# Kernel optimization log

Hardware: AMD Instinct MI355X
Metric: run time of the kernel (lower is better)

## Reference

```python
import jax, jax.numpy as jnp
import numpy as np

B, L, H, NHEADS = 32, 1024, 128, 2
HEAD = H // NHEADS
NEG = -2.0**32 + 1.0  # padding value used by the torch module


def setup_inputs() -> dict:
    key = jax.random.key(0)
    ks = jax.random.split(key, 9)
    queries = jax.random.normal(ks[0], (B, L, H), dtype=jnp.float32)
    keys = jax.random.normal(ks[1], (B, L, H), dtype=jnp.float32)
    time_mask = jax.random.bernoulli(ks[2], 0.1, (B, L))
    # causal mask: True above the diagonal (future positions masked)
    attn_mask = jnp.triu(jnp.ones((L, L), dtype=bool), k=1)
    s = 1.0 / np.sqrt(H)
    Qw = jax.random.uniform(ks[3], (H, H), jnp.float32, -s, s)
    Qb = jax.random.uniform(ks[4], (H,), jnp.float32, -s, s)
    Kw = jax.random.uniform(ks[5], (H, H), jnp.float32, -s, s)
    Kb = jax.random.uniform(ks[6], (H,), jnp.float32, -s, s)
    Vw = jax.random.uniform(ks[7], (H, H), jnp.float32, -s, s)
    Vb = jax.random.uniform(ks[8], (H,), jnp.float32, -s, s)
    return {"queries": queries, "keys": keys, "time_mask": time_mask,
            "attn_mask": attn_mask, "Qw": Qw, "Qb": Qb, "Kw": Kw, "Kb": Kb,
            "Vw": Vw, "Vb": Vb}


def reference(queries, keys, time_mask, attn_mask, Qw, Qb, Kw, Kb, Vw, Vb):
    b, l, h = queries.shape
    d = h // NHEADS
    # torch Linear: x @ W.T + b
    Q = queries @ Qw.T + Qb
    K = keys @ Kw.T + Kb
    V = keys @ Vw.T + Vb
    # split heads: torch cat(split(dim=2), dim=0) == (h, B, L, d) layout;
    # equivalent per-head math with (B, h, L, d):
    Qh = Q.reshape(b, l, NHEADS, d).transpose(0, 2, 1, 3)  # bhld
    Kh = K.reshape(b, l, NHEADS, d).transpose(0, 2, 1, 3)
    Vh = V.reshape(b, l, NHEADS, d).transpose(0, 2, 1, 3)
    scores = jnp.einsum('bhqd,bhkd->bhqk', Qh, Kh) / jnp.sqrt(
        jnp.asarray(d, dtype=Qh.dtype))
    # time_mask masks whole query rows; attn_mask is causal over (q, k)
    scores = jnp.where(time_mask[:, None, :, None], NEG, scores)
    scores = jnp.where(attn_mask[None, None, :, :], NEG, scores)
    attn = jax.nn.softmax(scores, axis=-1)  # dropout_rate=0 -> identity
    out = jnp.einsum('bhqk,bhkd->bhqd', attn, Vh)
    return out.transpose(0, 2, 1, 3).reshape(b, l, h)
```

## Files before the change

kernel.cpp:

```cpp
#include <hip/hip_runtime.h>

#define LSEQ 1024
#define DH 64
#define NH 2

typedef __attribute__((ext_vector_type(8))) __bf16 bf16x8;
typedef __attribute__((ext_vector_type(4))) float f32x4;
typedef __attribute__((ext_vector_type(8))) unsigned short ushort8;

__device__ __forceinline__ unsigned short f2bf(float f) {
  unsigned u = __float_as_uint(f);
  u += 0x7FFFu + ((u >> 16) & 1u);
  return (unsigned short)(u >> 16);
}
__device__ __forceinline__ unsigned cvt_pk_bf16(float lo, float hi) {
  unsigned r;
  asm("v_cvt_pk_bf16_f32 %0, %1, %2" : "=v"(r) : "v"(lo), "v"(hi));
  return r;
}
__device__ __forceinline__ void gload16(const void* g, void* l) {
  __builtin_amdgcn_global_load_lds(
      (const __attribute__((address_space(1))) void*)g,
      (__attribute__((address_space(3))) void*)l, 16, 0, 0);
}

#define QSCALE 0.1803368801111601f

__global__ __launch_bounds__(256) void wconv_kernel(
    const float* __restrict__ Qw, const float* __restrict__ Kw,
    const float* __restrict__ Vw, unsigned short* __restrict__ Wbf,
    float* __restrict__ Vmean)
{
  for (int i = blockIdx.x * 256 + threadIdx.x; i < NH * 32 * DH; i += 768)
    Vmean[i] = 0.f;
  const float* W = (blockIdx.x == 0) ? Qw : (blockIdx.x == 1) ? Kw : Vw;
  unsigned short* o = Wbf + blockIdx.x * 16384;
  const float4* W4 = (const float4*)W;
#pragma unroll
  for (int i = 0; i < 16; ++i) {
    const int idx = threadIdx.x + i * 256;
    const float4 v = W4[idx];
    uint2 u;
    u.x = cvt_pk_bf16(v.x, v.y);
    u.y = cvt_pk_bf16(v.z, v.w);
    *(uint2*)&o[idx * 4] = u;
  }
}

__global__ __launch_bounds__(256, 2) void proj_kernel(
    const float* __restrict__ queries, const float* __restrict__ keys,
    const unsigned short* __restrict__ Wbf,
    const float* __restrict__ Qb, const float* __restrict__ Kb,
    const float* __restrict__ Vb,
    unsigned short* __restrict__ Qbf, unsigned short* __restrict__ Kbf,
    unsigned short* __restrict__ Vt, float* __restrict__ Vmean)
{
  constexpr int LP = 136;
  __shared__ __align__(16) unsigned short Xs[128 * LP];
  __shared__ __align__(16) unsigned short Ws[16384];

  const int t = threadIdx.x;
  const int lane = t & 63, w = t >> 6;
  const int c = lane & 15, g = lane >> 4;
  const int wrow = w * 32;

  const int mat = blockIdx.x & 1;
  const int rt  = (blockIdx.x >> 1) * 128;

  const float* Xin = mat ? keys : queries;

#define WSTAGE(wi) do {                                                    \
    const char* Wg_ = (const char*)(Wbf + (wi) * 16384);                   \
    _Pragma("unroll")                                                      \
    for (int i_ = 0; i_ < 8; ++i_) {                                       \
      const int off_ = t * 16 + i_ * 4096;                                 \
      const int sch_ = ((((off_ >> 4) & 15) ^ ((off_ >> 8) & 7)) << 4);    \
      gload16(Wg_ + (off_ & ~0xFF) + sch_,                                 \
              (char*)Ws + w * 1024 + i_ * 4096);                           \
    }                                                                      \
  } while (0)

#define WFRAG(ct_, kc_) \
  (*(const bf16x8*)&Ws[((ct_) * 16 + c) * 128 + ((((kc_) * 4 + g) ^ (c & 7)) << 3)])

#define XFRAG(half_, kc_) \
  (*(const bf16x8*)&Xs[(wrow + (half_) * 16 + c) * LP + (kc_) * 32 + g * 8])

  WSTAGE(mat);

  const float4* X4 = (const float4*)(Xin + (size_t)rt * 128);
#pragma unroll
  for (int i = 0; i < 16; ++i) {
    const int e4 = t + i * 256;
    const float4 v = X4[e4];
    const int e = e4 * 4;
    uint2 u;
    u.x = cvt_pk_bf16(v.x, v.y);
    u.y = cvt_pk_bf16(v.z, v.w);
    *(uint2*)&Xs[(e >> 7) * LP + (e & 127)] = u;
  }
  __syncthreads();

  f32x4 accA[2][8];
#pragma unroll
  for (int i = 0; i < 2; ++i)
#pragma unroll
    for (int j = 0; j < 8; ++j) accA[i][j] = (f32x4){0.f, 0.f, 0.f, 0.f};

#pragma unroll
  for (int kc = 0; kc < 4; ++kc) {
    const bf16x8 a0 = XFRAG(0, kc);
    const bf16x8 a1 = XFRAG(1, kc);
#pragma unroll
    for (int ct = 0; ct < 8; ++ct) {
      const bf16x8 bfr = WFRAG(ct, kc);
      accA[0][ct] = __builtin_amdgcn_mfma_f32_16x16x32_bf16(a0, bfr, accA[0][ct], 0, 0, 0);
      accA[1][ct] = __builtin_amdgcn_mfma_f32_16x16x32_bf16(a1, bfr, accA[1][ct], 0, 0, 0);
    }
  }

  f32x4 accB[2][8];
  if (mat) {
    __syncthreads();
    WSTAGE(2);
    __syncthreads();

#pragma unroll
    for (int i = 0; i < 2; ++i)
#pragma unroll
      for (int j = 0; j < 8; ++j) accB[i][j] = (f32x4){0.f, 0.f, 0.f, 0.f};

#pragma unroll
    for (int kc = 0; kc < 4; ++kc) {
      const bf16x8 a0 = XFRAG(0, kc);
      const bf16x8 a1 = XFRAG(1, kc);
#pragma unroll
      for (int ct = 0; ct < 8; ++ct) {
        const bf16x8 bfr = WFRAG(ct, kc);
        accB[0][ct] = __builtin_amdgcn_mfma_f32_16x16x32_bf16(a0, bfr, accB[0][ct], 0, 0, 0);
        accB[1][ct] = __builtin_amdgcn_mfma_f32_16x16x32_bf16(a1, bfr, accB[1][ct], 0, 0, 0);
      }
    }

#pragma unroll
    for (int ct = 0; ct < 8; ++ct) {
      const float bv = Vb[ct * 16 + c];
      float cs = 8.f * bv;
#pragma unroll
      for (int qf = 0; qf < 2; ++qf)
#pragma unroll
        for (int r = 0; r < 4; ++r) cs += accB[qf][ct][r];
      cs += __shfl_xor(cs, 16);
      cs += __shfl_xor(cs, 32);
      if (g == 0) {
        const int col = ct * 16 + c;
        const int bh = (rt >> 10) * NH + (col >> 6);
        atomicAdd(&Vmean[bh * DH + (col & 63)], cs);
      }
    }
  }

  __syncthreads();
  {
    const float* biasA = mat ? Kb : Qb;
    const float qs = mat ? 1.0f : QSCALE;
#pragma unroll
    for (int qf = 0; qf < 2; ++qf)
#pragma unroll
      for (int ct = 0; ct < 8; ++ct) {
        const float bv = biasA[ct * 16 + c];
#pragma unroll
        for (int r = 0; r < 4; ++r)
          Xs[(wrow + qf * 16 + g * 4 + r) * LP + ct * 16 + c] =
              f2bf((accA[qf][ct][r] + bv) * qs);
      }
  }
  __syncthreads();
  {
    unsigned short* outp = (mat ? Kbf : Qbf) + (size_t)rt * 128;
#pragma unroll
    for (int i = 0; i < 8; ++i) {
      const int e = i * 2048 + t * 8;
      *(ushort8*)&outp[e] = *(const ushort8*)&Xs[(e >> 7) * LP + (e & 127)];
    }
  }

  if (mat) {
    __syncthreads();
#pragma unroll
    for (int qf = 0; qf < 2; ++qf)
#pragma unroll
      for (int ct = 0; ct < 8; ++ct) {
        const float bv = Vb[ct * 16 + c];
        const int col = ct * 16 + c;
        uint2 u;
        u.x = cvt_pk_bf16(accB[qf][ct][0] + bv, accB[qf][ct][1] + bv);
        u.y = cvt_pk_bf16(accB[qf][ct][2] + bv, accB[qf][ct][3] + bv);
        *(uint2*)&Xs[col * LP + wrow + qf * 16 + g * 4] = u;
      }
    __syncthreads();
    const int b = rt >> 10, l0 = rt & 1023;
#pragma unroll
    for (int i = 0; i < 8; ++i) {
      const int e = i * 2048 + t * 8;
      const int col = e >> 7, li = e & 127;
      const ushort8 v8 = *(const ushort8*)&Xs[col * LP + li];
      const int hh = col >> 6, dh = col & 63;
      unsigned short* vp = Vt + ((size_t)(b * NH + hh)) * (DH * LSEQ) +
                           (size_t)dh * LSEQ + l0 + li;
      *(ushort8*)vp = v8;
    }
  }
#undef WSTAGE
#undef WFRAG
#undef XFRAG
}

__global__ __launch_bounds__(256, 3) void attn_kernel(
    const unsigned short* __restrict__ Qbf, const unsigned short* __restrict__ Kbf,
    const unsigned short* __restrict__ Vt, const float* __restrict__ Vmean,
    const int* __restrict__ time_mask, float* __restrict__ out)
{
  __shared__ __align__(16) unsigned short smem[24576];

  const int tid = threadIdx.x;
  const int lane = tid & 63, w = tid >> 6;
  const int c = lane & 15, g = lane >> 4;

  const int wgid = blockIdx.x;
  const int xcd = wgid & 7;
  const int idx = wgid >> 3;
  const int bh  = xcd * 8 + (idx & 7);
  const int qb  = 7 - (idx >> 3);
  const int qbase = qb * 128;
  const int b = bh >> 1, h = bh & 1;

  const unsigned short* Qp = Qbf + ((size_t)b * LSEQ) * 128 + h * 64;
  const char* Kpb = (const char*)(Kbf + ((size_t)b * LSEQ) * 128 + h * 64);
  const char* Vpb = (const char*)(Vt + (size_t)bh * (DH * LSEQ));

  const int nkv = qb * 2 + 2;
  const int tkmax = qb * 2 + (w >> 1);

#define STAGE(tkv, bi) do {                                                   \
    const int kv_ = (tkv) * 64;                                               \
    _Pragma("unroll")                                                         \
    for (int r_ = 0; r_ < 2; ++r_) {                                          \
      const int off_ = tid * 16 + r_ * 4096;                                  \
      const int row_ = off_ >> 7;                                             \
      const int chk_ = (((off_ >> 4) & 7) ^ (row_ & 7)) << 4;                 \
      gload16(Kpb + (size_t)(kv_ + row_) * 256 + chk_,                        \
              (char*)smem + (bi) * 8192 + w * 1024 + r_ * 4096);              \
      gload16(Vpb + (size_t)row_ * 2048 + kv_ * 2 + chk_,                     \
              (char*)smem + 16384 + (bi) * 8192 + w * 1024 + r_ * 4096);      \
    }                                                                         \
  } while (0)

  bf16x8 qa[2][2];
#pragma unroll
  for (int qf = 0; qf < 2; ++qf)
#pragma unroll
    for (int kc = 0; kc < 2; ++kc)
      qa[qf][kc] = *(const bf16x8*)&Qp[(qbase + w * 32 + qf * 16 + c) * 128 + kc * 32 + g * 8];

  const __bf16 one = (__bf16)1.0f;
  const bf16x8 vones = {one, one, one, one, one, one, one, one};

  f32x4 acc[2][4];
  f32x4 acc5[2];
#pragma unroll
  for (int qf = 0; qf < 2; ++qf) {
    acc5[qf] = (f32x4){0.f, 0.f, 0.f, 0.f};
#pragma unroll
    for (int i = 0; i < 4; ++i) acc[qf][i] = (f32x4){0.f, 0.f, 0.f, 0.f};
  }

  unsigned short* const Pw = smem + 16384 + w * 2048;
  const int swz = (c & 7) << 3;

  STAGE(0, 0);
  __syncthreads();

  for (int tk = 0; tk < nkv; ++tk) {
    const int cur = tk & 1;
    if (tk + 1 < nkv) STAGE(tk + 1, cur ^ 1);

    if (tk <= tkmax) {
      const unsigned short* Kl = smem + cur * 4096;
      const unsigned short* Vl = smem + 8192 + cur * 4096;

      bf16x8 kb[4][2], vb[4][2];
#pragma unroll
      for (int sub = 0; sub < 4; ++sub)
#pragma unroll
        for (int kc = 0; kc < 2; ++kc)
          kb[sub][kc] = *(const bf16x8*)&Kl[(sub * 16 + c) * 64 + (((kc * 4 + g) << 3) ^ swz)];
#pragma unroll
      for (int dc = 0; dc < 4; ++dc)
#pragma unroll
        for (int kc = 0; kc < 2; ++kc)
          vb[dc][kc] = *(const bf16x8*)&Vl[(dc * 16 + c) * 64 + (((kc * 4 + g) << 3) ^ swz)];

      f32x4 s[2][4];
#pragma unroll
      for (int qf = 0; qf < 2; ++qf)
#pragma unroll
        for (int sub = 0; sub < 4; ++sub) {
          s[qf][sub] = __builtin_amdgcn_mfma_f32_16x16x32_bf16(
              kb[sub][0], qa[qf][0], (f32x4){0.f, 0.f, 0.f, 0.f}, 0, 0, 0);
          s[qf][sub] = __builtin_amdgcn_mfma_f32_16x16x32_bf16(
              kb[sub][1], qa[qf][1], s[qf][sub], 0, 0, 0);
        }

      const bool maskedT = (tk == tkmax);
      const int kv = tk * 64;
#pragma unroll
      for (int qf = 0; qf < 2; ++qf) {
        const int qrow = qbase + w * 32 + qf * 16 + c;
#pragma unroll
        for (int sub = 0; sub < 4; ++sub) {
          float p[4];
          if (maskedT) {
            const int key0 = kv + sub * 16 + g * 4;
#pragma unroll
            for (int r = 0; r < 4; ++r)
              p[r] = (key0 + r > qrow) ? 0.f : __builtin_amdgcn_exp2f(s[qf][sub][r]);
          } else {
#pragma unroll
            for (int r = 0; r < 4; ++r) p[r] = __builtin_amdgcn_exp2f(s[qf][sub][r]);
          }
          uint2 u;
          u.x = cvt_pk_bf16(p[0], p[1]);
          u.y = cvt_pk_bf16(p[2], p[3]);
          *(uint2*)&Pw[(qf * 16 + c) * 64 + ((sub * 16 + g * 4) ^ swz)] = u;
        }
      }

      bf16x8 pa[2][2];
#pragma unroll
      for (int qf = 0; qf < 2; ++qf)
#pragma unroll
        for (int kc = 0; kc < 2; ++kc)
          pa[qf][kc] = *(const bf16x8*)&Pw[(qf * 16 + c) * 64 + ((kc * 32 + g * 8) ^ swz)];

#pragma unroll
      for (int qf = 0; qf < 2; ++qf) {
        acc5[qf] = __builtin_amdgcn_mfma_f32_16x16x32_bf16(pa[qf][0], vones, acc5[qf], 0, 0, 0);
        acc5[qf] = __builtin_amdgcn_mfma_f32_16x16x32_bf16(pa[qf][1], vones, acc5[qf], 0, 0, 0);
#pragma unroll
        for (int dc = 0; dc < 4; ++dc) {
          acc[qf][dc] = __builtin_amdgcn_mfma_f32_16x16x32_bf16(pa[qf][0], vb[dc][0], acc[qf][dc], 0, 0, 0);
          acc[qf][dc] = __builtin_amdgcn_mfma_f32_16x16x32_bf16(pa[qf][1], vb[dc][1], acc[qf][dc], 0, 0, 0);
        }
      }
    }

    __syncthreads();
  }

#pragma unroll
  for (int qf = 0; qf < 2; ++qf)
#pragma unroll
    for (int r = 0; r < 4; ++r) {
      const int qrow = qbase + w * 32 + qf * 16 + g * 4 + r;
      const int tm = time_mask[b * LSEQ + qrow];
      const float inv = 1.0f / acc5[qf][r];
      float* orow = out + ((size_t)(b * LSEQ + qrow)) * (NH * DH) + h * DH;
      const float* vm = Vmean + bh * DH;
#pragma unroll
      for (int dc = 0; dc < 4; ++dc)
        orow[dc * 16 + c] = tm ? vm[dc * 16 + c] * (1.0f / 1024.0f)
                               : acc[qf][dc][r] * inv;
    }
#undef STAGE
}

extern "C" void kernel_launch(void* const* d_in, const int* in_sizes, int n_in,
                              void* d_out, int out_size, void* d_ws, size_t ws_size,
                              hipStream_t stream) {
  const float* queries   = (const float*)d_in[0];
  const float* keys      = (const float*)d_in[1];
  const int*   time_mask = (const int*)d_in[2];
  const float* Qw = (const float*)d_in[4];
  const float* Qb = (const float*)d_in[5];
  const float* Kw = (const float*)d_in[6];
  const float* Kb = (const float*)d_in[7];
  const float* Vw = (const float*)d_in[8];
  const float* Vb = (const float*)d_in[9];
  float* out = (float*)d_out;

  char* ws = (char*)d_ws;
  unsigned short* Wbf   = (unsigned short*)(ws);
  float*          Vmean = (float*)(ws + 98304);
  unsigned short* Qbf   = (unsigned short*)(ws + 114688);
  unsigned short* Kbf   = (unsigned short*)(ws + 8503296);
  unsigned short* Vtp   = (unsigned short*)(ws + 16891904);

  wconv_kernel<<<3, 256, 0, stream>>>(Qw, Kw, Vw, Wbf, Vmean);
  proj_kernel<<<512, 256, 0, stream>>>(queries, keys, Wbf, Qb, Kb, Vb,
                                       Qbf, Kbf, Vtp, Vmean);
  attn_kernel<<<512, 256, 0, stream>>>(Qbf, Kbf, Vtp, Vmean, time_mask, out);
}
```

Measured before the change: 53.54 us.

## Switch attention to 32x32x16 MFMA with register-resident P via permlane32 swap

The attention inner loop moves from 16x16x32 to 32x32x16 bf16 MFMA tiles. The probability matrix is repacked in registers with v_permlane32_swap instead of a round trip through LDS, and the row-sum is kept as a scalar accumulator instead of an extra MFMA against a ones vector. The epilogue reduces the row sum across lane halves and passes the inverse through a small LDS scratch. Occupancy hint drops from 3 to 2 blocks to leave room for the larger accumulators, at the risk of less latency hiding.

```diff
diff --git a/kernel.cpp b/kernel.cpp
--- a/kernel.cpp
+++ b/kernel.cpp
@@ -6,6 +6,8 @@
 
 typedef __attribute__((ext_vector_type(8))) __bf16 bf16x8;
 typedef __attribute__((ext_vector_type(4))) float f32x4;
+typedef __attribute__((ext_vector_type(16))) float f32x16;
+typedef __attribute__((ext_vector_type(4))) unsigned u32x4;
 typedef __attribute__((ext_vector_type(8))) unsigned short ushort8;
 
 __device__ __forceinline__ unsigned short f2bf(float f) {
@@ -216,16 +218,17 @@
 #undef XFRAG
 }
 
-__global__ __launch_bounds__(256, 3) void attn_kernel(
+__global__ __launch_bounds__(256, 2) void attn_kernel(
     const unsigned short* __restrict__ Qbf, const unsigned short* __restrict__ Kbf,
     const unsigned short* __restrict__ Vt, const float* __restrict__ Vmean,
     const int* __restrict__ time_mask, float* __restrict__ out)
 {
-  __shared__ __align__(16) unsigned short smem[24576];
+  __shared__ __align__(16) char smem[33280];
 
   const int tid = threadIdx.x;
   const int lane = tid & 63, w = tid >> 6;
-  const int c = lane & 15, g = lane >> 4;
+  const int lq = lane & 31, hi = lane >> 5;
+  const int s7 = lq & 7;
 
   const int wgid = blockIdx.x;
   const int xcd = wgid & 7;
@@ -256,27 +259,23 @@
     }                                                                         \
   } while (0)
 
-  bf16x8 qa[2][2];
-#pragma unroll
-  for (int qf = 0; qf < 2; ++qf)
-#pragma unroll
-    for (int kc = 0; kc < 2; ++kc)
-      qa[qf][kc] = *(const bf16x8*)&Qp[(qbase + w * 32 + qf * 16 + c) * 128 + kc * 32 + g * 8];
-
-  const __bf16 one = (__bf16)1.0f;
-  const bf16x8 vones = {one, one, one, one, one, one, one, one};
-
-  f32x4 acc[2][4];
-  f32x4 acc5[2];
-#pragma unroll
-  for (int qf = 0; qf < 2; ++qf) {
-    acc5[qf] = (f32x4){0.f, 0.f, 0.f, 0.f};
-#pragma unroll
-    for (int i = 0; i < 4; ++i) acc[qf][i] = (f32x4){0.f, 0.f, 0.f, 0.f};
-  }
-
-  unsigned short* const Pw = smem + 16384 + w * 2048;
-  const int swz = (c & 7) << 3;
+#define PLSWAP(x_, y_) asm("v_permlane32_swap_b32 %0, %1" : "+v"(x_), "+v"(y_))
+
+#define MKPA(pk_, m_, dst_) do {                                              \
+    unsigned x0_ = pk_[4*(m_)], x1_ = pk_[4*(m_)+1];                          \
+    unsigned y0_ = pk_[4*(m_)+2], y1_ = pk_[4*(m_)+3];                        \
+    PLSWAP(x0_, y0_); PLSWAP(x1_, y1_);                                       \
+    u32x4 u_ = {x0_, x1_, y0_, y1_};                                          \
+    dst_ = *(bf16x8*)&u_;                                                     \
+  } while (0)
+
+  bf16x8 qa[4];
+#pragma unroll
+  for (int kc4 = 0; kc4 < 4; ++kc4)
+    qa[kc4] = *(const bf16x8*)&Qp[(qbase + w * 32 + lq) * 128 + kc4 * 16 + hi * 8];
+
+  f32x16 acc0 = {}, acc1 = {};
+  float lsum = 0.f;
 
   STAGE(0, 0);
   __syncthreads();
@@ -286,93 +285,103 @@
     if (tk + 1 < nkv) STAGE(tk + 1, cur ^ 1);
 
     if (tk <= tkmax) {
-      const unsigned short* Kl = smem + cur * 4096;
-      const unsigned short* Vl = smem + 8192 + cur * 4096;
-
-      bf16x8 kb[4][2], vb[4][2];
-#pragma unroll
-      for (int sub = 0; sub < 4; ++sub)
-#pragma unroll
-        for (int kc = 0; kc < 2; ++kc)
-          kb[sub][kc] = *(const bf16x8*)&Kl[(sub * 16 + c) * 64 + (((kc * 4 + g) << 3) ^ swz)];
-#pragma unroll
-      for (int dc = 0; dc < 4; ++dc)
-#pragma unroll
-        for (int kc = 0; kc < 2; ++kc)
-          vb[dc][kc] = *(const bf16x8*)&Vl[(dc * 16 + c) * 64 + (((kc * 4 + g) << 3) ^ swz)];
-
-      f32x4 s[2][4];
-#pragma unroll
-      for (int qf = 0; qf < 2; ++qf)
-#pragma unroll
-        for (int sub = 0; sub < 4; ++sub) {
-          s[qf][sub] = __builtin_amdgcn_mfma_f32_16x16x32_bf16(
-              kb[sub][0], qa[qf][0], (f32x4){0.f, 0.f, 0.f, 0.f}, 0, 0, 0);
-          s[qf][sub] = __builtin_amdgcn_mfma_f32_16x16x32_bf16(
-              kb[sub][1], qa[qf][1], s[qf][sub], 0, 0, 0);
+      const char* Kl = smem + cur * 8192;
+      const char* Vl = smem + 16384 + cur * 8192;
+
+      f32x16 s0 = {}, s1 = {};
+#pragma unroll
+      for (int kc4 = 0; kc4 < 4; ++kc4) {
+        const bf16x8 kf = *(const bf16x8*)(Kl + (lq << 7) + (((2 * kc4 + hi) ^ s7) << 4));
+        s0 = __builtin_amdgcn_mfma_f32_32x32x16_bf16(kf, qa[kc4], s0, 0, 0, 0);
+      }
+#pragma unroll
+      for (int kc4 = 0; kc4 < 4; ++kc4) {
+        const bf16x8 kf = *(const bf16x8*)(Kl + ((32 + lq) << 7) + (((2 * kc4 + hi) ^ s7) << 4));
+        s1 = __builtin_amdgcn_mfma_f32_32x32x16_bf16(kf, qa[kc4], s1, 0, 0, 0);
+      }
+
+      bf16x8 vf[4][2];
+#pragma unroll
+      for (int kc4 = 0; kc4 < 4; ++kc4)
+#pragma unroll
+        for (int dt = 0; dt < 2; ++dt)
+          vf[kc4][dt] = *(const bf16x8*)(Vl + ((dt * 32 + lq) << 7) + (((2 * kc4 + hi) ^ s7) << 4));
+
+      const bool diag = (tk == tkmax);
+      const int kv = tk * 64;
+      const int qrow = qbase + w * 32 + lq;
+      float p0[16], p1[16];
+#pragma unroll
+      for (int r = 0; r < 16; ++r) {
+        const int krow = (r & 3) + 8 * (r >> 2) + 4 * hi;
+        float e0 = __builtin_amdgcn_exp2f(s0[r]);
+        float e1 = __builtin_amdgcn_exp2f(s1[r]);
+        if (diag) {
+          if (kv + krow > qrow)      e0 = 0.f;
+          if (kv + 32 + krow > qrow) e1 = 0.f;
         }
-
-      const bool maskedT = (tk == tkmax);
-      const int kv = tk * 64;
-#pragma unroll
-      for (int qf = 0; qf < 2; ++qf) {
-        const int qrow = qbase + w * 32 + qf * 16 + c;
-#pragma unroll
-        for (int sub = 0; sub < 4; ++sub) {
-          float p[4];
-          if (maskedT) {
-            const int key0 = kv + sub * 16 + g * 4;
-#pragma unroll
-            for (int r = 0; r < 4; ++r)
-              p[r] = (key0 + r > qrow) ? 0.f : __builtin_amdgcn_exp2f(s[qf][sub][r]);
-          } else {
-#pragma unroll
-            for (int r = 0; r < 4; ++r) p[r] = __builtin_amdgcn_exp2f(s[qf][sub][r]);
-          }
-          uint2 u;
-          u.x = cvt_pk_bf16(p[0], p[1]);
-          u.y = cvt_pk_bf16(p[2], p[3]);
-          *(uint2*)&Pw[(qf * 16 + c) * 64 + ((sub * 16 + g * 4) ^ swz)] = u;
-        }
-      }
-
-      bf16x8 pa[2][2];
-#pragma unroll
-      for (int qf = 0; qf < 2; ++qf)
-#pragma unroll
-        for (int kc = 0; kc < 2; ++kc)
-          pa[qf][kc] = *(const bf16x8*)&Pw[(qf * 16 + c) * 64 + ((kc * 32 + g * 8) ^ swz)];
-
-#pragma unroll
-      for (int qf = 0; qf < 2; ++qf) {
-        acc5[qf] = __builtin_amdgcn_mfma_f32_16x16x32_bf16(pa[qf][0], vones, acc5[qf], 0, 0, 0);
-        acc5[qf] = __builtin_amdgcn_mfma_f32_16x16x32_bf16(pa[qf][1], vones, acc5[qf], 0, 0, 0);
-#pragma unroll
-        for (int dc = 0; dc < 4; ++dc) {
-          acc[qf][dc] = __builtin_amdgcn_mfma_f32_16x16x32_bf16(pa[qf][0], vb[dc][0], acc[qf][dc], 0, 0, 0);
-          acc[qf][dc] = __builtin_amdgcn_mfma_f32_16x16x32_bf16(pa[qf][1], vb[dc][1], acc[qf][dc], 0, 0, 0);
-        }
-      }
+        p0[r] = e0; p1[r] = e1;
+        lsum += e0 + e1;
+      }
+
+      unsigned pk0[8], pk1[8];
+#pragma unroll
+      for (int bb = 0; bb < 4; ++bb) {
+        pk0[2*bb]   = cvt_pk_bf16(p0[4*bb],   p0[4*bb+1]);
+        pk0[2*bb+1] = cvt_pk_bf16(p0[4*bb+2], p0[4*bb+3]);
+        pk1[2*bb]   = cvt_pk_bf16(p1[4*bb],   p1[4*bb+1]);
+        pk1[2*bb+1] = cvt_pk_bf16(p1[4*bb+2], p1[4*bb+3]);
+      }
+
+      bf16x8 pa;
+      MKPA(pk0, 0, pa);
+      acc0 = __builtin_amdgcn_mfma_f32_32x32x16_bf16(pa, vf[0][0], acc0, 0, 0, 0);
+      acc1 = __builtin_amdgcn_mfma_f32_32x32x16_bf16(pa, vf[0][1], acc1, 0, 0, 0);
+      MKPA(pk0, 1, pa);
+      acc0 = __builtin_amdgcn_mfma_f32_32x32x16_bf16(pa, vf[1][0], acc0, 0, 0, 0);
+      acc1 = __builtin_amdgcn_mfma_f32_32x32x16_bf16(pa, vf[1][1], acc1, 0, 0, 0);
+      MKPA(pk1, 0, pa);
+      acc0 = __builtin_amdgcn_mfma_f32_32x32x16_bf16(pa, vf[2][0], acc0, 0, 0, 0);
+      acc1 = __builtin_amdgcn_mfma_f32_32x32x16_bf16(pa, vf[2][1], acc1, 0, 0, 0);
+      MKPA(pk1, 1, pa);
+      acc0 = __builtin_amdgcn_mfma_f32_32x32x16_bf16(pa, vf[3][0], acc0, 0, 0, 0);
+      acc1 = __builtin_amdgcn_mfma_f32_32x32x16_bf16(pa, vf[3][1], acc1, 0, 0, 0);
     }
 
     __syncthreads();
   }
 
-#pragma unroll
-  for (int qf = 0; qf < 2; ++qf)
-#pragma unroll
-    for (int r = 0; r < 4; ++r) {
-      const int qrow = qbase + w * 32 + qf * 16 + g * 4 + r;
-      const int tm = time_mask[b * LSEQ + qrow];
-      const float inv = 1.0f / acc5[qf][r];
-      float* orow = out + ((size_t)(b * LSEQ + qrow)) * (NH * DH) + h * DH;
-      const float* vm = Vmean + bh * DH;
-#pragma unroll
-      for (int dc = 0; dc < 4; ++dc)
-        orow[dc * 16 + c] = tm ? vm[dc * 16 + c] * (1.0f / 1024.0f)
-                               : acc[qf][dc][r] * inv;
-    }
+  float pa_ = lsum, pb_ = lsum;
+  PLSWAP(pa_, pb_);
+  const float total = lsum + (hi ? pa_ : pb_);
+
+  float* lsx = (float*)(smem + 32768 + w * 128);
+  if (hi == 0) {
+    const int tm = time_mask[b * LSEQ + qbase + w * 32 + lq];
+    lsx[lq] = tm ? -1.0f : 1.0f / total;
+  }
+  asm volatile("s_waitcnt lgkmcnt(0)" ::: "memory");
+  __builtin_amdgcn_sched_barrier(0);
+
+  f32x4 inv4[4];
+#pragma unroll
+  for (int bb = 0; bb < 4; ++bb)
+    inv4[bb] = *(const f32x4*)&lsx[8 * bb + 4 * hi];
+
+  const float vmv0 = Vmean[bh * DH + lq]      * (1.0f / 1024.0f);
+  const float vmv1 = Vmean[bh * DH + 32 + lq] * (1.0f / 1024.0f);
+
+#pragma unroll
+  for (int r = 0; r < 16; ++r) {
+    const int qr = (r & 3) + 8 * (r >> 2) + 4 * hi;
+    const float wv = inv4[r >> 2][r & 3];
+    float* orow = out + (size_t)(b * LSEQ + qbase + w * 32 + qr) * (NH * DH) + h * DH;
+    orow[lq]      = (wv < 0.f) ? vmv0 : acc0[r] * wv;
+    orow[32 + lq] = (wv < 0.f) ? vmv1 : acc1[r] * wv;
+  }
 #undef STAGE
+#undef PLSWAP
+#undef MKPA
 }
 
 extern "C" void kernel_launch(void* const* d_in, const int* in_sizes, int n_in,
```

New measurement: 49.90 us. 1.07x faster.
